# Optimization experiments

Measured on AMD Instinct MI355X. Metric: run time of the kernel, lower is better.

Reference implementation:

```python
import jax, jax.numpy as jnp
import numpy as np

N, K, HC, NH, VD, NAA, AC, L = 8192, 30, 64, 8, 8, 20, 91, 4
EPS = 1e-7

def _normalize(v):
    return v / jnp.sqrt(jnp.sum(v * v, -1, keepdims=True) + EPS)

def _dihedrals(bb):
    # bb [N,4,3]; chain of N,Ca,C atoms -> phi/psi/omega -> cos/sin features [N,6]
    X = bb[:, :3].reshape(-1, 3)
    U = _normalize(X[1:] - X[:-1])
    u2, u1, u0 = U[:-2], U[1:-1], U[2:]
    n2 = _normalize(jnp.cross(u2, u1))
    n1 = _normalize(jnp.cross(u1, u0))
    cosD = jnp.clip(jnp.sum(n2 * n1, -1), -1 + EPS, 1 - EPS)
    D = jnp.sign(jnp.sum(u2 * n1, -1)) * jnp.arccos(cosD)
    D = jnp.pad(D, (1, 2)).reshape(-1, 3)
    return jnp.concatenate([jnp.cos(D), jnp.sin(D)], -1)

def _orientations(X):
    f = jnp.pad(_normalize(X[1:] - X[:-1]), ((0, 1), (0, 0)))
    b = jnp.pad(_normalize(X[:-1] - X[1:]), ((1, 0), (0, 0)))
    return jnp.stack([f, b], -2)  # [N,2,3]

def _virtual_cb(bb):
    # ideal virtual C-beta relative to Ca
    b = bb[:, 1] - bb[:, 0]
    c = bb[:, 2] - bb[:, 1]
    a = jnp.cross(b, c)
    return -0.58273431 * a + 0.56802827 * b - 0.54067466 * c

def _rbf(d, d_count=16, d_max=20.0):
    mu = jnp.linspace(0.0, d_max, d_count)
    sigma = d_max / d_count
    return jnp.exp(-(((d[..., None] - mu) / sigma) ** 2))

def _pos_emb(src, num_emb=16):
    d = (src - jnp.arange(src.shape[0])[:, None]).astype(jnp.float32)
    freq = jnp.exp(jnp.arange(0, num_emb, 2, dtype=jnp.float32) * (-np.log(10000.0) / num_emb))
    ang = d[..., None] * freq
    return jnp.concatenate([jnp.cos(ang), jnp.sin(ang)], -1)

def _edge_rot_mat(vec):
    # rotation taking world frame -> edge-aligned frame (rows x,y,z)
    z = _normalize(vec)
    ex = jnp.array([1.0, 0.0, 0.0]); ey = jnp.array([0.0, 1.0, 0.0])
    ref = jnp.where(jnp.abs(z[..., :1]) < 0.9, ex, ey)
    x = _normalize(ref - jnp.sum(ref * z, -1, keepdims=True) * z)
    y = jnp.cross(z, x)
    return jnp.stack([x, y, z], -2)

def _knn(X):
    d2 = jnp.sum((X[:, None, :] - X[None, :, :]) ** 2, -1)  # [N,N]
    i = jnp.arange(X.shape[0])
    d2 = d2.at[i, i].set(jnp.inf)
    return jax.lax.top_k(-d2, K)[1]  # [N,K] source (neighbor) ids per target

def _so3_conv(x, ef, src, R, Wrad, brad, Wgate, W0, W1):
    # equivariant edge conv: gather, rotate l=1 into edge frame, channel-mix,
    # gate by radial MLP of edge features, rotate back, aggregate over K neighbors
    xs = x[src]                                              # [N,K,4,Cin]
    s1 = jnp.einsum('nkij,nkjc->nkic', R, xs[:, :, 1:4])
    m0 = xs[:, :, 0] @ W0
    m1 = jnp.einsum('nkic,co->nkio', s1, W1)
    g0, g1 = jnp.split(jax.nn.silu(ef @ Wrad + brad) @ Wgate, 2, -1)
    m1 = jnp.einsum('nkji,nkjc->nkic', R, m1 * g1[:, :, None, :])
    return jnp.concatenate([jnp.sum(m0 * g0, 1)[:, None], jnp.sum(m1, 1)], 1) / np.sqrt(K)

def _attn(x, ef, src, R, Walpha, Wv0, Wv1, Wo):
    # SO2/SO3 graph attention: invariant alpha over K neighbors, equivariant values
    x0 = x[:, 0]
    feat = jnp.concatenate([x0[src], jnp.broadcast_to(x0[:, None], (N, K, x0.shape[-1])), ef], -1)
    a = jax.nn.softmax(jax.nn.leaky_relu(feat @ Walpha, 0.2), axis=1)  # [N,K,NH]
    xs = x[src]
    s1 = jnp.einsum('nkij,nkjc->nkic', R, xs[:, :, 1:4])
    v0 = (xs[:, :, 0] @ Wv0).reshape(N, K, NH, VD)
    v1 = jnp.einsum('nkic,ch->nkih', s1, Wv1).reshape(N, K, 3, NH, VD)
    o0 = jnp.sum(v0 * a[..., None], 1).reshape(N, NH * VD)
    v1 = (v1 * a[:, :, None, :, None]).reshape(N, K, 3, NH * VD)
    o1 = jnp.sum(jnp.einsum('nkji,nkjc->nkic', R, v1), 1)
    return jnp.concatenate([o0[:, None], o1], 1) @ Wo

def _ffn(x, W1, W2):
    t = x[:, 0] @ W1
    h1 = jnp.einsum('nic,ch->nih', x[:, 1:4], W1) * jax.nn.sigmoid(t)[:, None, :]
    return jnp.concatenate([(jax.nn.silu(t) @ W2)[:, None], jnp.einsum('nih,ho->nio', h1, W2)], 1)

def _forward(bb, seq, latent, eb_Wrad, eb_brad, eb_Wgate, eb_W0, eb_W1, t_Walpha, t_Wv0, t_Wv1, t_Wo, t_Wf1, t_Wf2, e_W, e_b, p_Walpha, p_Wv0, p_Wv1, p_Wo, p_Wf1, p_Wf2, oa_Wrad, oa_brad, oa_Wgate, oa_W0, oa_W1, ln_g, ln_b, W_seq, b_seq, src):
    X_ca = bb[:, 1]
    vec = X_ca[src] - X_ca[:, None]                     # [N,K,3]
    R = _edge_rot_mat(vec)
    dist = jnp.sqrt(jnp.sum(vec * vec, -1) + EPS)
    ef = jnp.concatenate([_rbf(dist), _pos_emb(src)], -1)  # [N,K,32]
    # bb SO3 embedding: l=0 -> dihedrals + seq one-hot (masked to zero per noising_mask);
    # l=1 -> 7 relative vectors (4 bb_rel, 2 orientations, 1 virtual Cb), zero-padded to 26 ch
    scal = jnp.concatenate([_dihedrals(bb), jnp.zeros((N, NAA), bb.dtype)], -1)
    vecs = jnp.nan_to_num(jnp.concatenate([bb - X_ca[:, None], _orientations(X_ca), _virtual_cb(bb)[:, None]], 1))
    l1 = jnp.zeros((N, 3, scal.shape[-1]), bb.dtype).at[:, :, :7].set(jnp.transpose(vecs, (0, 2, 1)))
    bbemb = jnp.concatenate([scal[:, None], l1], 1)     # [N,4,26]
    bbout = _so3_conv(bbemb, ef, src, R, eb_Wrad, eb_brad, eb_Wgate, eb_W0, eb_W1)  # [N,4,32]
    res = jnp.concatenate([bbout, latent], -1)          # [N,4,64]
    for i in range(L):
        res = res + _attn(res, ef, src, R, t_Walpha[i], t_Wv0[i], t_Wv1[i], t_Wo[i])
        res = res + _ffn(res, t_Wf1[i], t_Wf2[i])
        efeat = jnp.concatenate([res[:, 0][src], jnp.broadcast_to(res[:, 0][:, None], (N, K, HC)), ef], -1)
        ef = jnp.tanh(efeat @ e_W[i] + e_b[i])
    p = _attn(res, ef, src, R, p_Walpha, p_Wv0, p_Wv1, p_Wo)  # [N,4,32]
    p = p + _ffn(p, p_Wf1, p_Wf2)
    atoms = _so3_conv(p, ef, src, R, oa_Wrad, oa_brad, oa_Wgate, oa_W0, oa_W1)  # [N,4,91]
    inv = atoms[:, 0]
    mu = jnp.mean(inv, -1, keepdims=True)
    var = jnp.var(inv, -1, keepdims=True)
    logits = jax.nn.log_softmax(((inv - mu) / jnp.sqrt(var + 1e-5) * ln_g + ln_b) @ W_seq + b_seq, -1)
    decoded = jnp.transpose(atoms[:, 1:4], (0, 2, 1))   # [N,91,3]
    return decoded, logits

def setup_inputs():
    key = jax.random.key(0)
    ks = jax.random.split(key, 30)
    def p(k, shape, fan):
        return jax.random.normal(k, shape, jnp.float32) * (fan ** -0.5)
    ca = jnp.cumsum(jax.random.normal(ks[0], (N, 3)) * 2.2, 0)
    bb = ca[:, None, :] + jax.random.normal(ks[1], (N, 4, 3)) * 0.8
    CA160 = 2 * HC + 32
    return {
        'bb': bb,
        'seq': jax.random.randint(ks[2], (N,), 0, NAA),
        'latent': jax.random.normal(ks[3], (N, 4, HC // 2)),
        'eb_Wrad': p(ks[4], (32, 64), 32), 'eb_brad': jnp.zeros((64,)),
        'eb_Wgate': p(ks[5], (64, 64), 64), 'eb_W0': p(ks[6], (26, 32), 26), 'eb_W1': p(ks[7], (26, 32), 26),
        't_Walpha': p(ks[8], (L, CA160, NH), CA160),
        't_Wv0': p(ks[9], (L, HC, NH * VD), HC), 't_Wv1': p(ks[10], (L, HC, NH * VD), HC),
        't_Wo': p(ks[11], (L, NH * VD, HC), NH * VD),
        't_Wf1': p(ks[12], (L, HC, HC), HC), 't_Wf2': p(ks[13], (L, HC, HC), HC),
        'e_W': p(ks[14], (L, CA160, 32), CA160), 'e_b': jnp.zeros((L, 32)),
        'p_Walpha': p(ks[15], (CA160, NH), CA160),
        'p_Wv0': p(ks[16], (HC, NH * VD), HC), 'p_Wv1': p(ks[17], (HC, NH * VD), HC),
        'p_Wo': p(ks[18], (NH * VD, 32), NH * VD),
        'p_Wf1': p(ks[19], (32, 32), 32), 'p_Wf2': p(ks[20], (32, 32), 32),
        'oa_Wrad': p(ks[21], (32, 64), 32), 'oa_brad': jnp.zeros((64,)),
        'oa_Wgate': p(ks[22], (64, 2 * AC), 64), 'oa_W0': p(ks[23], (32, AC), 32), 'oa_W1': p(ks[24], (32, AC), 32),
        'ln_g': jnp.ones((AC,)), 'ln_b': jnp.zeros((AC,)),
        'W_seq': p(ks[25], (AC, NAA), AC), 'b_seq': jnp.zeros((NAA,)),
    }

def reference(bb, seq, latent, eb_Wrad, eb_brad, eb_Wgate, eb_W0, eb_W1, t_Walpha, t_Wv0, t_Wv1, t_Wo, t_Wf1, t_Wf2, e_W, e_b, p_Walpha, p_Wv0, p_Wv1, p_Wo, p_Wf1, p_Wf2, oa_Wrad, oa_brad, oa_Wgate, oa_W0, oa_W1, ln_g, ln_b, W_seq, b_seq):
    src = _knn(bb[:, 1])
    return _forward(bb, seq, latent, eb_Wrad, eb_brad, eb_Wgate, eb_W0, eb_W1, t_Walpha, t_Wv0, t_Wv1, t_Wo, t_Wf1, t_Wf2, e_W, e_b, p_Walpha, p_Wv0, p_Wv1, p_Wo, p_Wf1, p_Wf2, oa_Wrad, oa_brad, oa_Wgate, oa_W0, oa_W1, ln_g, ln_b, W_seq, b_seq, src)
```

## Files before the change

### kernel.cpp

```cpp
#include <hip/hip_runtime.h>
#include <math.h>


#define NN 8192
#define KK 30
#define NE (NN*KK)
#define EPSF 1e-7f

static const size_t O_SRC = 0;
static const size_t O_XS  = 1ull<<20;
static const size_t O_YS  = O_XS + (size_t)NN*4;
static const size_t O_ZS  = O_XS + (size_t)NN*8;
static const size_t O_BBE = 2ull<<20;
static const size_t O_RES = 6ull<<20;
static const size_t O_P   = 15ull<<20;
static const size_t O_EF  = 20ull<<20;
static const size_t O_NF  = 52ull<<20;
static const size_t O_V1  = 55ull<<20;
static const size_t O_O   = 62ull<<20;
static const size_t O_EE  = 71ull<<20;
static const size_t O_M0E = 52ull<<20;
static const size_t O_M1E = 54ull<<20;
static const size_t O_M0O = 52ull<<20;
static const size_t O_M1O = 56ull<<20;
static const size_t O_ATM = 6ull<<20;
static const size_t WS_NEEDED = 80ull<<20;

__device__ __forceinline__ float nn0(float v){ return (v != v) ? 0.f : v; }
__device__ __forceinline__ void norm3(float& x, float& y, float& z){
  float s = sqrtf(x*x + y*y + z*z + EPSF);
  x /= s; y /= s; z /= s;
}

__global__ void k_prep(const float* __restrict__ bb, float* __restrict__ xs,
                       float* __restrict__ ys, float* __restrict__ zs,
                       float* __restrict__ bbe){
  int n = blockIdx.x*blockDim.x + threadIdx.x;
  if (n >= NN) return;
  const float* bn = bb + (size_t)n*12;
  float a0x=bn[0],a0y=bn[1],a0z=bn[2];
  float cax=bn[3],cay=bn[4],caz=bn[5];
  float a2x=bn[6],a2y=bn[7],a2z=bn[8];
  float a3x=bn[9],a3y=bn[10],a3z=bn[11];
  xs[n]=cax; ys[n]=cay; zs[n]=caz;
  float v[7][3];
  v[0][0]=a0x-cax; v[0][1]=a0y-cay; v[0][2]=a0z-caz;
  v[1][0]=0.f;     v[1][1]=0.f;     v[1][2]=0.f;
  v[2][0]=a2x-cax; v[2][1]=a2y-cay; v[2][2]=a2z-caz;
  v[3][0]=a3x-cax; v[3][1]=a3y-cay; v[3][2]=a3z-caz;
  if (n < NN-1){
    float fx=bb[(size_t)(n+1)*12+3]-cax, fy=bb[(size_t)(n+1)*12+4]-cay, fz=bb[(size_t)(n+1)*12+5]-caz;
    norm3(fx,fy,fz); v[4][0]=fx; v[4][1]=fy; v[4][2]=fz;
  } else { v[4][0]=v[4][1]=v[4][2]=0.f; }
  if (n > 0){
    float gx=bb[(size_t)(n-1)*12+3]-cax, gy=bb[(size_t)(n-1)*12+4]-cay, gz=bb[(size_t)(n-1)*12+5]-caz;
    norm3(gx,gy,gz); v[5][0]=gx; v[5][1]=gy; v[5][2]=gz;
  } else { v[5][0]=v[5][1]=v[5][2]=0.f; }
  {
    float bx=cax-a0x, by=cay-a0y, bz=caz-a0z;
    float cx=a2x-cax, cy=a2y-cay, cz=a2z-caz;
    float ax = by*cz - bz*cy, ay = bz*cx - bx*cz, az = bx*cy - by*cx;
    v[6][0] = -0.58273431f*ax + 0.56802827f*bx - 0.54067466f*cx;
    v[6][1] = -0.58273431f*ay + 0.56802827f*by - 0.54067466f*cy;
    v[6][2] = -0.58273431f*az + 0.56802827f*bz - 0.54067466f*cz;
  }
  float* be = bbe + (size_t)n*104;
  #pragma unroll
  for (int c=6;c<26;++c) be[c]=0.f;
  #pragma unroll
  for (int s=0;s<3;++s){
    float* br = be + 26*(1+s);
    #pragma unroll
    for (int c=0;c<26;++c) br[c] = (c<7) ? nn0(v[c][s]) : 0.f;
  }
}

__global__ void k_dihed(const float* __restrict__ bb, float* __restrict__ bbe){
  int t = blockIdx.x*blockDim.x + threadIdx.x;
  if (t >= 3*NN) return;
  float cD = 1.f, sD = 0.f;
  if (t >= 1 && t < 3*NN-2){
    int i = t-1;
    float p[4][3];
    #pragma unroll
    for (int m=0;m<4;++m){
      int a = i+m; int rn = a/3, ra = a - rn*3;
      const float* q = bb + (size_t)(rn*4 + ra)*3;
      p[m][0]=q[0]; p[m][1]=q[1]; p[m][2]=q[2];
    }
    float u2x=p[1][0]-p[0][0], u2y=p[1][1]-p[0][1], u2z=p[1][2]-p[0][2];
    float u1x=p[2][0]-p[1][0], u1y=p[2][1]-p[1][1], u1z=p[2][2]-p[1][2];
    float u0x=p[3][0]-p[2][0], u0y=p[3][1]-p[2][1], u0z=p[3][2]-p[2][2];
    norm3(u2x,u2y,u2z); norm3(u1x,u1y,u1z); norm3(u0x,u0y,u0z);
    float n2x=u2y*u1z-u2z*u1y, n2y=u2z*u1x-u2x*u1z, n2z=u2x*u1y-u2y*u1x;
    float n1x=u1y*u0z-u1z*u0y, n1y=u1z*u0x-u1x*u0z, n1z=u1x*u0y-u1y*u0x;
    norm3(n2x,n2y,n2z); norm3(n1x,n1y,n1z);
    float cosD = n2x*n1x + n2y*n1y + n2z*n1z;
    const float lo = (float)(-1.0 + 1e-7), hi = (float)(1.0 - 1e-7);
    cosD = fminf(fmaxf(cosD, lo), hi);
    float sg = u2x*n1x + u2y*n1y + u2z*n1z;
    float sgn = (sg > 0.f) ? 1.f : ((sg < 0.f) ? -1.f : 0.f);
    float D = sgn * acosf(cosD);
    cD = cosf(D); sD = sinf(D);
  }
  int n = t/3, col = t - n*3;
  bbe[(size_t)n*104 + col] = cD;
  bbe[(size_t)n*104 + 3 + col] = sD;
}

__global__ __launch_bounds__(256) void k_knn(const float* __restrict__ xs,
        const float* __restrict__ ys, const float* __restrict__ zs, int* __restrict__ src){
  __shared__ float sd[4][32];
  __shared__ int   si[4][32];
  int w = threadIdx.x >> 6, lane = threadIdx.x & 63;
  int n = blockIdx.x*4 + w;
  float qx = xs[n], qy = ys[n], qz = zs[n];
  if (lane >= 30 && lane < 32){ sd[w][lane] = INFINITY; si[w][lane] = 0; }

  int w0 = n - 32; if (w0 < 0) w0 = 0; if (w0 > NN-64) w0 = NN-64;
  int idx = w0 + lane;
  {
    float dx = qx - xs[idx], dy = qy - ys[idx], dz = qz - zs[idx];
    float d2 = dx*dx + dy*dy + dz*dz;
    if (idx == n) d2 = INFINITY;
    #pragma unroll
    for (int k = 2; k <= 64; k <<= 1){
      #pragma unroll
      for (int jj = k>>1; jj >= 1; jj >>= 1){
        float od = __shfl_xor(d2, jj);
        int   oi = __shfl_xor(idx, jj);
        bool up      = ((lane & k) == 0);
        bool lower   = ((lane & jj) == 0);
        bool takeMin = (up == lower);
        bool mless   = (d2 < od) || (d2 == od && idx < oi);
        if (mless != takeMin){ d2 = od; idx = oi; }
      }
    }
    if (lane < 30){ sd[w][lane] = d2; si[w][lane] = idx; }
  }
  float thr = sd[w][29];

  for (int s = 0; s < NN/64; ++s){
    int j = s*64 + lane;
    float dx = __fsub_rn(qx, xs[j]);
    float dy = __fsub_rn(qy, ys[j]);
    float dz = __fsub_rn(qz, zs[j]);
    float d2 = __fadd_rn(__fadd_rn(__fmul_rn(dx,dx),__fmul_rn(dy,dy)),__fmul_rn(dz,dz));
    if (j == n) d2 = INFINITY;
    if (j >= w0 && j < w0+64) d2 = INFINITY;
    unsigned long long bal = __ballot(d2 < thr);
    if (bal){
      while (bal){
        int b = __ffsll((unsigned long long)bal) - 1;
        bal &= bal - 1ull;
        float vd = __shfl(d2, b);
        int vj = s*64 + b;
        float dl = 0.f; int il = 0; bool keep = true;
        if (lane < 30){ dl = sd[w][lane]; il = si[w][lane]; keep = (dl <= vd); }
        unsigned long long km = __ballot(lane < 30 && keep);
        int pos = __popcll(km);
        if (lane < 30 && !keep){ sd[w][lane+1] = dl; si[w][lane+1] = il; }
        if (lane == pos){ sd[w][lane] = vd; si[w][lane] = vj; }
      }
      thr = sd[w][29];
    }
  }
  if (lane < 30) src[(size_t)n*KK + lane] = si[w][lane];
}

__global__ void k_edgefeat(const int* __restrict__ src, const float* __restrict__ xs,
        const float* __restrict__ ys, const float* __restrict__ zs, float* __restrict__ ef){
  int e = blockIdx.x*blockDim.x + threadIdx.x;
  if (e >= NE) return;
  int n = e / KK;
  int j = src[e];
  float vx = xs[j]-xs[n], vy = ys[j]-ys[n], vz = zs[j]-zs[n];
  float dist = sqrtf(vx*vx + vy*vy + vz*vz + EPSF);
  float* o = ef + (size_t)e*32;
  #pragma unroll
  for (int m=0;m<16;++m){
    float mu = (float)m * (20.f/15.f);
    float q = (dist - mu) / 1.25f;
    o[m] = expf(-q*q);
  }
  float d = (float)(j - n);
  const float Cf = -0.5756462732485115f;
  #pragma unroll
  for (int fi=0; fi<8; ++fi){
    float fr = expf((float)(2*fi) * Cf);
    float ang = d * fr;
    o[16+fi] = cosf(ang);
    o[24+fi] = sinf(ang);
  }
}

template<int K, int ACT, int BSEL>
__global__ __launch_bounds__(256) void k_gemm(const float* __restrict__ A,
        const float* __restrict__ B1, const float* __restrict__ B2,
        const float* __restrict__ bias, float* __restrict__ C,
        int M, int Nc, int arpg, int agst, int arst, int aoff, int beta){
  __shared__ float As[64*(K+1)];
  __shared__ alignas(16) float Bs[K*64];
  int tid = threadIdx.x, tm = blockIdx.x, tn = blockIdx.y;
  for (int i = tid; i < K*64; i += 256){
    int kk = i >> 6, cl = i & 63;
    int c = tn*64 + cl;
    float v = 0.f;
    if (c < Nc){
      if (BSEL == 0) v = B1[kk*Nc + c];
      else if (BSEL == 1) v = (c<8) ? B1[kk*8+c] : ((c<16) ? B1[(64+kk)*8 + (c-8)] : B2[kk*64 + (c-16)]);
      else v = (c<32) ? B1[kk*32 + c] : B1[(64+kk)*32 + (c-32)];
    }
    Bs[i] = v;
  }
  for (int i = tid; i < 64*K; i += 256){
    int rl = i / K, kk = i - rl*K;
    int r = tm*64 + rl;
    float v = 0.f;
    if (r < M){
      const float* ap;
      if (arpg == 1) ap = A + (size_t)r*agst + aoff;
      else { int g = r/3; int wr = r - g*3; ap = A + (size_t)g*agst + wr*arst + aoff; }
      v = ap[kk];
    }
    As[rl*(K+1) + kk] = v;
  }
  __syncthreads();
  int tx = tid & 15, ty = tid >> 4;
  float acc[4][4] = {};
  for (int kk = 0; kk < K; ++kk){
    float4 b4 = *reinterpret_cast<const float4*>(&Bs[kk*64 + tx*4]);
    #pragma unroll
    for (int rr = 0; rr < 4; ++rr){
      float a = As[(ty*4+rr)*(K+1) + kk];
      acc[rr][0] += a*b4.x; acc[rr][1] += a*b4.y; acc[rr][2] += a*b4.z; acc[rr][3] += a*b4.w;
    }
  }
  if (ACT == 2){
    int r0 = tm*64 + ty*4;
    #pragma unroll
    for (int cc = 0; cc < 4; ++cc){
      int c = tn*64 + tx*4 + cc;
      if (c >= Nc) continue;
      float t0 = acc[0][cc];
      float g = 1.f/(1.f + expf(-t0));
      C[(size_t)(r0+0)*Nc + c] = t0*g;
      C[(size_t)(r0+1)*Nc + c] = acc[1][cc]*g;
      C[(size_t)(r0+2)*Nc + c] = acc[2][cc]*g;
      C[(size_t)(r0+3)*Nc + c] = acc[3][cc]*g;
    }
  } else {
    #pragma unroll
    for (int rr = 0; rr < 4; ++rr){
      int r = tm*64 + ty*4 + rr;
      if (r >= M) continue;
      #pragma unroll
      for (int cc = 0; cc < 4; ++cc){
        int c = tn*64 + tx*4 + cc;
        if (c >= Nc) continue;
        float v = acc[rr][cc];
        if (bias) v += bias[c];
        size_t ci = (size_t)r*Nc + c;
        if (beta) v += C[ci];
        C[ci] = v;
      }
    }
  }
}

__global__ __launch_bounds__(256) void k_attn(const int* __restrict__ src,
        const float* __restrict__ NF, const float* __restrict__ V1,
        const float* __restrict__ ef, const float* __restrict__ WaE, float* __restrict__ o){
  int w = threadIdx.x >> 6, lane = threadIdx.x & 63;
  int n = blockIdx.x*4 + w;
  int h = lane >> 3, q = lane & 7;
  float w0 = WaE[(q*4+0)*8 + h];
  float w1 = WaE[(q*4+1)*8 + h];
  float w2 = WaE[(q*4+2)*8 + h];
  float w3 = WaE[(q*4+3)*8 + h];
  const int* sk = src + (size_t)n*KK;
  int myj = (lane < KK) ? sk[lane] : 0;
  float a2 = NF[(size_t)n*80 + 8 + h];
  float m = -INFINITY, s = 0.f, o0=0.f, o1=0.f, o2=0.f, o3=0.f;
  for (int k = 0; k < KK; ++k){
    int j = __shfl(myj, k);
    float4 e4 = *reinterpret_cast<const float4*>(ef + ((size_t)n*KK + k)*32 + q*4);
    float val = e4.x*w0 + e4.y*w1 + e4.z*w2 + e4.w*w3;
    val += __shfl_xor(val, 1);
    val += __shfl_xor(val, 2);
    val += __shfl_xor(val, 4);
    float l = val + NF[(size_t)j*80 + h] + a2;
    l = (l >= 0.f) ? l : 0.2f*l;
    float mn = fmaxf(m, l);
    float f = expf(m - mn);
    float pp = expf(l - mn);
    s = s*f + pp;
    const float* v1p = V1 + (size_t)j*192;
    o0 = o0*f + pp*NF[(size_t)j*80 + 16 + lane];
    o1 = o1*f + pp*v1p[lane];
    o2 = o2*f + pp*v1p[64+lane];
    o3 = o3*f + pp*v1p[128+lane];
    m = mn;
  }
  float inv = 1.f/s;
  float* op = o + (size_t)n*256;
  op[lane] = o0*inv; op[64+lane] = o1*inv; op[128+lane] = o2*inv; op[192+lane] = o3*inv;
}

template<int C>
__global__ __launch_bounds__(256) void k_so3fused(const int* __restrict__ src,
        const float* __restrict__ ef, const float* __restrict__ Wrad,
        const float* __restrict__ brad, const float* __restrict__ Wgate,
        const float* __restrict__ M0, const float* __restrict__ M1,
        float* __restrict__ out, int nstr, int sstr){
  constexpr int KG  = 256 / C;
  constexpr int KPT = (KK + KG - 1) / KG;
  __shared__ float efs[KK*32];
  __shared__ float Wr[32*64];
  __shared__ float Hs[KK*64];
  __shared__ float Wg[64*(C+1)];
  __shared__ float part[3*256];
  __shared__ int   js[KK];
  int n = blockIdx.x, tid = threadIdx.x;
  for (int i = tid; i < KK*32; i += 256) efs[i] = ef[(size_t)n*KK*32 + i];
  for (int i = tid; i < 2048;  i += 256) Wr[i]  = Wrad[i];
  if (tid < KK) js[tid] = src[(size_t)n*KK + tid];
  __syncthreads();
  for (int i = tid; i < KK*64; i += 256){
    int k = i >> 6, h = i & 63;
    float a = brad[h];
    const float* er = efs + k*32;
    #pragma unroll
    for (int m = 0; m < 32; ++m) a += er[m]*Wr[m*64 + h];
    Hs[i] = a/(1.f + expf(-a));
  }
  __syncthreads();
  int c = tid % C, kg = tid / C;
  bool act = (kg < KG);
  for (int i = tid; i < 64*C; i += 256){ int m = i/C, cc = i - m*C; Wg[m*(C+1)+cc] = Wgate[m*2*C + cc]; }
  __syncthreads();
  if (act){
    float a0 = 0.f;
    for (int t = 0; t < KPT; ++t){
      int k = kg*KPT + t;
      if (k < KK){
        const float* hr = Hs + k*64;
        float g = 0.f;
        #pragma unroll
        for (int m = 0; m < 64; ++m) g += hr[m]*Wg[m*(C+1) + c];
        a0 += g * M0[(size_t)js[k]*C + c];
      }
    }
    part[kg*C + c] = a0;
  }
  __syncthreads();
  const float IS = 0.18257418583505536f;
  if (tid < C){
    float s = 0.f;
    for (int g = 0; g < KG; ++g) s += part[g*C + tid];
    out[(size_t)n*nstr + tid] = s*IS;
  }
  __syncthreads();
  for (int i = tid; i < 64*C; i += 256){ int m = i/C, cc = i - m*C; Wg[m*(C+1)+cc] = Wgate[m*2*C + C + cc]; }
  __syncthreads();
  if (act){
    float a1 = 0.f, a2 = 0.f, a3 = 0.f;
    for (int t = 0; t < KPT; ++t){
      int k = kg*KPT + t;
      if (k < KK){
        const float* hr = Hs + k*64;
        float g = 0.f;
        #pragma unroll
        for (int m = 0; m < 64; ++m) g += hr[m]*Wg[m*(C+1) + c];
        const float* m1p = M1 + (size_t)js[k]*3*C;
        a1 += g*m1p[c]; a2 += g*m1p[C+c]; a3 += g*m1p[2*C+c];
      }
    }
    part[kg*C + c] = a1;
    part[KG*C + kg*C + c] = a2;
    part[2*KG*C + kg*C + c] = a3;
  }
  __syncthreads();
  if (tid < C){
    float s1=0.f, s2=0.f, s3=0.f;
    for (int g = 0; g < KG; ++g){
      s1 += part[g*C + tid];
      s2 += part[KG*C + g*C + tid];
      s3 += part[2*KG*C + g*C + tid];
    }
    float* ob = out + (size_t)n*nstr + tid;
    ob[sstr] = s1*IS; ob[2*sstr] = s2*IS; ob[3*sstr] = s3*IS;
  }
}

__global__ void k_lat(const float* __restrict__ latent, float* __restrict__ res){
  int t = blockIdx.x*blockDim.x + threadIdx.x;
  if (t >= NN*128) return;
  int n = t >> 7, rc = t & 127, s = rc >> 5, c = rc & 31;
  res[(size_t)n*256 + s*64 + 32 + c] = latent[t];
}

__global__ __launch_bounds__(256) void k_edgeout(const int* __restrict__ src,
        const float* __restrict__ eWe, const float* __restrict__ EE,
        const float* __restrict__ ebv, float* __restrict__ ef){
  __shared__ float ws[32*32];
  __shared__ float es[8*32];
  int tid = threadIdx.x;
  size_t e0 = (size_t)blockIdx.x*8;
  for (int i = tid; i < 1024; i += 256) ws[i] = eWe[i];
  es[tid] = ef[e0*32 + tid];
  __syncthreads();
  int le = tid >> 5, c = tid & 31;
  size_t e = e0 + le;
  int n = (int)(e / KK);
  int j = src[e];
  float acc = ebv[c] + EE[(size_t)j*64 + c] + EE[(size_t)n*64 + 32 + c];
  const float* er = es + le*32;
  #pragma unroll
  for (int kk = 0; kk < 32; ++kk) acc += er[kk]*ws[kk*32 + c];
  ef[e*32 + c] = tanhf(acc);
}

__global__ __launch_bounds__(128) void k_head(const float* __restrict__ atoms,
        const float* __restrict__ ln_g, const float* __restrict__ ln_b,
        const float* __restrict__ W_seq, const float* __restrict__ b_seq, float* __restrict__ out){
  __shared__ float red[128];
  __shared__ float nrm[91];
  __shared__ float lg[20];
  int n = blockIdx.x, t = threadIdx.x;
  const float* inv = atoms + (size_t)n*364;
  float x = (t < 91) ? inv[t] : 0.f;
  red[t] = x; __syncthreads();
  for (int off=64; off>=1; off>>=1){ if (t<off) red[t]+=red[t+off]; __syncthreads(); }
  float mu = red[0] / 91.f;
  __syncthreads();
  float d = x - mu;
  red[t] = (t<91) ? d*d : 0.f; __syncthreads();
  for (int off=64; off>=1; off>>=1){ if (t<off) red[t]+=red[t+off]; __syncthreads(); }
  float var = red[0] / 91.f;
  __syncthreads();
  if (t < 91) nrm[t] = (x - mu)/sqrtf(var + 1e-5f) * ln_g[t] + ln_b[t];
  __syncthreads();
  if (t < 20){
    float acc = b_seq[t];
    for (int c=0;c<91;++c) acc += nrm[c]*W_seq[c*20+t];
    lg[t] = acc;
  }
  __syncthreads();
  if (t == 0){
    float mx = lg[0];
    for (int i=1;i<20;++i) mx = fmaxf(mx, lg[i]);
    float s = 0.f;
    for (int i=0;i<20;++i) s += expf(lg[i]-mx);
    red[0] = mx + logf(s);
  }
  __syncthreads();
  float lse = red[0];
  if (t < 20) out[(size_t)NN*273 + (size_t)n*20 + t] = lg[t] - lse;
  for (int idx = t; idx < 273; idx += 128){
    int c = idx/3, i = idx - c*3;
    out[(size_t)n*273 + idx] = atoms[(size_t)n*364 + (1+i)*91 + c];
  }
}

static void gemm(hipStream_t st, int K, int act, int bsel, const float* A,
                 const float* B1, const float* B2, const float* bias, float* C,
                 int M, int Nc, int arpg, int agst, int arst, int aoff, int beta){
  dim3 g((M+63)/64, (Nc+63)/64), b(256);
  if (K == 26){
    k_gemm<26,0,0><<<g,b,0,st>>>(A,B1,B2,bias,C,M,Nc,arpg,agst,arst,aoff,beta);
  } else if (K == 32){
    if (act == 2) k_gemm<32,2,0><<<g,b,0,st>>>(A,B1,B2,bias,C,M,Nc,arpg,agst,arst,aoff,beta);
    else          k_gemm<32,0,0><<<g,b,0,st>>>(A,B1,B2,bias,C,M,Nc,arpg,agst,arst,aoff,beta);
  } else {
    if (act == 2)        k_gemm<64,2,0><<<g,b,0,st>>>(A,B1,B2,bias,C,M,Nc,arpg,agst,arst,aoff,beta);
    else if (bsel == 1)  k_gemm<64,0,1><<<g,b,0,st>>>(A,B1,B2,bias,C,M,Nc,arpg,agst,arst,aoff,beta);
    else if (bsel == 2)  k_gemm<64,0,2><<<g,b,0,st>>>(A,B1,B2,bias,C,M,Nc,arpg,agst,arst,aoff,beta);
    else                 k_gemm<64,0,0><<<g,b,0,st>>>(A,B1,B2,bias,C,M,Nc,arpg,agst,arst,aoff,beta);
  }
}

extern "C" void kernel_launch(void* const* d_in, const int* in_sizes, int n_in,
                              void* d_out, int out_size, void* d_ws, size_t ws_size,
                              hipStream_t stream){
  (void)in_sizes; (void)n_in; (void)out_size;
  if (ws_size < WS_NEEDED) return;

  const float* bb      = (const float*)d_in[0];
  const float* latent  = (const float*)d_in[2];
  const float* eb_Wrad = (const float*)d_in[3];
  const float* eb_brad = (const float*)d_in[4];
  const float* eb_Wgate= (const float*)d_in[5];
  const float* eb_W0   = (const float*)d_in[6];
  const float* eb_W1   = (const float*)d_in[7];
  const float* t_Walpha= (const float*)d_in[8];
  const float* t_Wv0   = (const float*)d_in[9];
  const float* t_Wv1   = (const float*)d_in[10];
  const float* t_Wo    = (const float*)d_in[11];
  const float* t_Wf1   = (const float*)d_in[12];
  const float* t_Wf2   = (const float*)d_in[13];
  const float* e_W     = (const float*)d_in[14];
  const float* e_b     = (const float*)d_in[15];
  const float* p_Walpha= (const float*)d_in[16];
  const float* p_Wv0   = (const float*)d_in[17];
  const float* p_Wv1   = (const float*)d_in[18];
  const float* p_Wo    = (const float*)d_in[19];
  const float* p_Wf1   = (const float*)d_in[20];
  const float* p_Wf2   = (const float*)d_in[21];
  const float* oa_Wrad = (const float*)d_in[22];
  const float* oa_brad = (const float*)d_in[23];
  const float* oa_Wgate= (const float*)d_in[24];
  const float* oa_W0   = (const float*)d_in[25];
  const float* oa_W1   = (const float*)d_in[26];
  const float* ln_g    = (const float*)d_in[27];
  const float* ln_b    = (const float*)d_in[28];
  const float* W_seq   = (const float*)d_in[29];
  const float* b_seq   = (const float*)d_in[30];

  char* w = (char*)d_ws;
  int*   src = (int*)  (w + O_SRC);
  float* xs  = (float*)(w + O_XS);
  float* ys  = (float*)(w + O_YS);
  float* zs  = (float*)(w + O_ZS);
  float* bbe = (float*)(w + O_BBE);
  float* res = (float*)(w + O_RES);
  float* p   = (float*)(w + O_P);
  float* ef  = (float*)(w + O_EF);
  float* NF  = (float*)(w + O_NF);
  float* V1  = (float*)(w + O_V1);
  float* o   = (float*)(w + O_O);
  float* EE  = (float*)(w + O_EE);
  float* M0e = (float*)(w + O_M0E);
  float* M1e = (float*)(w + O_M1E);
  float* M0o = (float*)(w + O_M0O);
  float* M1o = (float*)(w + O_M1O);
  float* atm = (float*)(w + O_ATM);

  k_prep <<<(NN+255)/256, 256, 0, stream>>>(bb, xs, ys, zs, bbe);
  k_dihed<<<(3*NN+255)/256, 256, 0, stream>>>(bb, bbe);
  k_knn  <<<NN/4, 256, 0, stream>>>(xs, ys, zs, src);
  k_edgefeat<<<(NE+255)/256, 256, 0, stream>>>(src, xs, ys, zs, ef);

  gemm(stream, 26,0,0, bbe, eb_W0, nullptr, nullptr, M0e, NN,   32, 1,104, 0, 0, 0);
  gemm(stream, 26,0,0, bbe, eb_W1, nullptr, nullptr, M1e, 3*NN, 32, 3,104,26,26, 0);
  k_so3fused<32><<<NN, 256, 0, stream>>>(src, ef, eb_Wrad, eb_brad, eb_Wgate, M0e, M1e, res, 256, 64);
  k_lat<<<(NN*128+255)/256, 256, 0, stream>>>(latent, res);

  for (int L=0; L<4; ++L){
    const float* Wa  = t_Walpha + (size_t)L*160*8;
    const float* Wv0 = t_Wv0 + (size_t)L*64*64;
    const float* Wv1 = t_Wv1 + (size_t)L*64*64;
    const float* Wo  = t_Wo  + (size_t)L*64*64;
    const float* Wf1 = t_Wf1 + (size_t)L*64*64;
    const float* Wf2 = t_Wf2 + (size_t)L*64*64;
    const float* eWl = e_W   + (size_t)L*160*32;
    const float* ebl = e_b   + (size_t)L*32;
    gemm(stream, 64,0,1, res, Wa, Wv0, nullptr, NF, NN,   80, 1,256, 0, 0, 0);
    gemm(stream, 64,0,0, res, Wv1, nullptr, nullptr, V1, 3*NN, 64, 3,256,64,64, 0);
    k_attn<<<NN/4, 256, 0, stream>>>(src, NF, V1, ef, Wa + 128*8, o);
    gemm(stream, 64,0,0, o,   Wo,  nullptr, nullptr, res, 4*NN, 64, 1,64,0,0, 1);
    gemm(stream, 64,2,0, res, Wf1, nullptr, nullptr, o,   4*NN, 64, 1,64,0,0, 0);
    gemm(stream, 64,0,0, o,   Wf2, nullptr, nullptr, res, 4*NN, 64, 1,64,0,0, 1);
    gemm(stream, 64,0,2, res, eWl, nullptr, nullptr, EE,  NN,   64, 1,256,0,0, 0);
    k_edgeout<<<NE/8, 256, 0, stream>>>(src, eWl + 128*32, EE, ebl, ef);
  }

  gemm(stream, 64,0,1, res, p_Walpha, p_Wv0, nullptr, NF, NN,   80, 1,256, 0, 0, 0);
  gemm(stream, 64,0,0, res, p_Wv1, nullptr, nullptr, V1, 3*NN, 64, 3,256,64,64, 0);
  k_attn<<<NN/4, 256, 0, stream>>>(src, NF, V1, ef, p_Walpha + 128*8, o);
  gemm(stream, 64,0,0, o, p_Wo,  nullptr, nullptr, p, 4*NN, 32, 1,64,0,0, 0);
  gemm(stream, 32,2,0, p, p_Wf1, nullptr, nullptr, o, 4*NN, 32, 1,32,0,0, 0);
  gemm(stream, 32,0,0, o, p_Wf2, nullptr, nullptr, p, 4*NN, 32, 1,32,0,0, 1);

  gemm(stream, 32,0,0, p, oa_W0, nullptr, nullptr, M0o, NN,   91, 1,128, 0, 0, 0);
  gemm(stream, 32,0,0, p, oa_W1, nullptr, nullptr, M1o, 3*NN, 91, 3,128,32,32, 0);
  k_so3fused<91><<<NN, 256, 0, stream>>>(src, ef, oa_Wrad, oa_brad, oa_Wgate, M0o, M1o, atm, 364, 91);

  k_head<<<NN, 128, 0, stream>>>(atm, ln_g, ln_b, W_seq, b_seq, (float*)d_out);
}
```

Before: 1.398 ms.

## Vectorize GEMM and SO3 conv inner loops with float4 register blocking

New measurement: 1.371 ms. 2.0% less time.

```diff
diff --git a/kernel.cpp b/kernel.cpp
--- a/kernel.cpp
+++ b/kernel.cpp
@@ -198,42 +198,52 @@
 __global__ __launch_bounds__(256) void k_gemm(const float* __restrict__ A,
         const float* __restrict__ B1, const float* __restrict__ B2,
         const float* __restrict__ bias, float* __restrict__ C,
-        int M, int Nc, int arpg, int agst, int arst, int aoff, int beta){
-  __shared__ float As[64*(K+1)];
-  __shared__ alignas(16) float Bs[K*64];
+        int M, int Nc, int ldc, int arpg, int agst, int arst, int aoff, int beta){
+  constexpr int KP = (K+3)&~3;
+  constexpr int SP = ((KP+4)%32==0) ? KP+8 : KP+4;
+  __shared__ alignas(16) float As[64*SP];
+  __shared__ alignas(16) float Bs[KP*64];
   int tid = threadIdx.x, tm = blockIdx.x, tn = blockIdx.y;
-  for (int i = tid; i < K*64; i += 256){
+  for (int i = tid; i < KP*64; i += 256){
     int kk = i >> 6, cl = i & 63;
     int c = tn*64 + cl;
     float v = 0.f;
-    if (c < Nc){
+    if (c < Nc && kk < K){
       if (BSEL == 0) v = B1[kk*Nc + c];
       else if (BSEL == 1) v = (c<8) ? B1[kk*8+c] : ((c<16) ? B1[(64+kk)*8 + (c-8)] : B2[kk*64 + (c-16)]);
       else v = (c<32) ? B1[kk*32 + c] : B1[(64+kk)*32 + (c-32)];
     }
     Bs[i] = v;
   }
-  for (int i = tid; i < 64*K; i += 256){
-    int rl = i / K, kk = i - rl*K;
+  for (int i = tid; i < 64*KP; i += 256){
+    int rl = i / KP, kk = i - rl*KP;
     int r = tm*64 + rl;
     float v = 0.f;
-    if (r < M){
+    if (r < M && kk < K){
       const float* ap;
       if (arpg == 1) ap = A + (size_t)r*agst + aoff;
       else { int g = r/3; int wr = r - g*3; ap = A + (size_t)g*agst + wr*arst + aoff; }
       v = ap[kk];
     }
-    As[rl*(K+1) + kk] = v;
+    As[rl*SP + kk] = v;
   }
   __syncthreads();
   int tx = tid & 15, ty = tid >> 4;
   float acc[4][4] = {};
-  for (int kk = 0; kk < K; ++kk){
-    float4 b4 = *reinterpret_cast<const float4*>(&Bs[kk*64 + tx*4]);
+  #pragma unroll 2
+  for (int kq = 0; kq < KP/4; ++kq){
+    float4 a0 = *reinterpret_cast<const float4*>(&As[(ty*4+0)*SP + kq*4]);
+    float4 a1 = *reinterpret_cast<const float4*>(&As[(ty*4+1)*SP + kq*4]);
+    float4 a2 = *reinterpret_cast<const float4*>(&As[(ty*4+2)*SP + kq*4]);
+    float4 a3 = *reinterpret_cast<const float4*>(&As[(ty*4+3)*SP + kq*4]);
     #pragma unroll
-    for (int rr = 0; rr < 4; ++rr){
-      float a = As[(ty*4+rr)*(K+1) + kk];
-      acc[rr][0] += a*b4.x; acc[rr][1] += a*b4.y; acc[rr][2] += a*b4.z; acc[rr][3] += a*b4.w;
+    for (int mm = 0; mm < 4; ++mm){
+      float4 b4 = *reinterpret_cast<const float4*>(&Bs[(kq*4+mm)*64 + tx*4]);
+      float e0 = (&a0.x)[mm], e1 = (&a1.x)[mm], e2 = (&a2.x)[mm], e3 = (&a3.x)[mm];
+      acc[0][0] += e0*b4.x; acc[0][1] += e0*b4.y; acc[0][2] += e0*b4.z; acc[0][3] += e0*b4.w;
+      acc[1][0] += e1*b4.x; acc[1][1] += e1*b4.y; acc[1][2] += e1*b4.z; acc[1][3] += e1*b4.w;
+      acc[2][0] += e2*b4.x; acc[2][1] += e2*b4.y; acc[2][2] += e2*b4.z; acc[2][3] += e2*b4.w;
+      acc[3][0] += e3*b4.x; acc[3][1] += e3*b4.y; acc[3][2] += e3*b4.z; acc[3][3] += e3*b4.w;
     }
   }
   if (ACT == 2){
@@ -244,10 +254,10 @@
       if (c >= Nc) continue;
       float t0 = acc[0][cc];
       float g = 1.f/(1.f + expf(-t0));
-      C[(size_t)(r0+0)*Nc + c] = t0*g;
-      C[(size_t)(r0+1)*Nc + c] = acc[1][cc]*g;
-      C[(size_t)(r0+2)*Nc + c] = acc[2][cc]*g;
-      C[(size_t)(r0+3)*Nc + c] = acc[3][cc]*g;
+      C[(size_t)(r0+0)*ldc + c] = t0*g;
+      C[(size_t)(r0+1)*ldc + c] = acc[1][cc]*g;
+      C[(size_t)(r0+2)*ldc + c] = acc[2][cc]*g;
+      C[(size_t)(r0+3)*ldc + c] = acc[3][cc]*g;
     }
   } else {
     #pragma unroll
@@ -260,7 +270,7 @@
         if (c >= Nc) continue;
         float v = acc[rr][cc];
         if (bias) v += bias[c];
-        size_t ci = (size_t)r*Nc + c;
+        size_t ci = (size_t)r*ldc + c;
         if (beta) v += C[ci];
         C[ci] = v;
       }
@@ -312,92 +322,124 @@
         const float* __restrict__ ef, const float* __restrict__ Wrad,
         const float* __restrict__ brad, const float* __restrict__ Wgate,
         const float* __restrict__ M0, const float* __restrict__ M1,
-        float* __restrict__ out, int nstr, int sstr){
-  constexpr int KG  = 256 / C;
-  constexpr int KPT = (KK + KG - 1) / KG;
-  __shared__ float efs[KK*32];
-  __shared__ float Wr[32*64];
-  __shared__ float Hs[KK*64];
-  __shared__ float Wg[64*(C+1)];
-  __shared__ float part[3*256];
-  __shared__ int   js[KK];
+        const float* __restrict__ lat, float* __restrict__ out, int nstr, int sstr){
+  constexpr int KT = (C==32) ? 2 : 4;
+  constexpr int KG = 32/KT;
+  constexpr int NQ = (C==32) ? 16 : 23;
+  constexpr int PW = (C==32) ? 32 : 92;
+  constexpr int CG = (C==32) ? 64 : 92;
+  constexpr int HS = 68;
+  constexpr int NPASS = (C==32) ? 1 : 2;
+  constexpr int NT = KG*NQ;
+  constexpr int LD0 = PW;
+  constexpr int LD1 = PW;
+  __shared__ alignas(16) float uni[64*CG];
+  __shared__ alignas(16) float Hs[32*HS];
+  __shared__ alignas(16) float part[4*KG*PW];
+  __shared__ int js[32];
+  float* efs = uni;
+  float* Wr  = uni + 30*32;
+  float* Wg  = uni;
   int n = blockIdx.x, tid = threadIdx.x;
   for (int i = tid; i < KK*32; i += 256) efs[i] = ef[(size_t)n*KK*32 + i];
   for (int i = tid; i < 2048;  i += 256) Wr[i]  = Wrad[i];
-  if (tid < KK) js[tid] = src[(size_t)n*KK + tid];
-  __syncthreads();
-  for (int i = tid; i < KK*64; i += 256){
+  if (tid < 32) js[tid] = (tid < KK) ? src[(size_t)n*KK + tid] : 0;
+  __syncthreads();
+  for (int i = tid; i < 32*64; i += 256){
     int k = i >> 6, h = i & 63;
-    float a = brad[h];
-    const float* er = efs + k*32;
+    float v = 0.f;
+    if (k < KK){
+      float a = brad[h];
+      const float* er = efs + k*32;
+      #pragma unroll
+      for (int m = 0; m < 32; ++m) a += er[m]*Wr[m*64 + h];
+      v = a/(1.f + expf(-a));
+    }
+    Hs[k*HS + h] = v;
+  }
+  int kg = tid / NQ, cq = tid - kg*NQ;
+  bool act = (tid < NT);
+  for (int pass = 0; pass < NPASS; ++pass){
+    __syncthreads();
+    for (int i = tid; i < 64*CG; i += 256){
+      int m = i/CG, u = i - m*CG;
+      float v = 0.f;
+      if (C == 32) v = Wgate[m*64 + u];
+      else if (u < 91) v = Wgate[m*182 + pass*91 + u];
+      Wg[i] = v;
+    }
+    __syncthreads();
+    if (act){
+      float g[KT][4];
+      #pragma unroll
+      for (int i=0;i<KT;++i){ g[i][0]=0.f; g[i][1]=0.f; g[i][2]=0.f; g[i][3]=0.f; }
+      #pragma unroll 2
+      for (int mq = 0; mq < 16; ++mq){
+        float4 hs[KT];
+        #pragma unroll
+        for (int i=0;i<KT;++i) hs[i] = *reinterpret_cast<const float4*>(&Hs[(kg*KT+i)*HS + mq*4]);
+        #pragma unroll
+        for (int mm=0; mm<4; ++mm){
+          float4 w4 = *reinterpret_cast<const float4*>(&Wg[(mq*4+mm)*CG + cq*4]);
+          #pragma unroll
+          for (int i=0;i<KT;++i){
+            float h = (&hs[i].x)[mm];
+            g[i][0] += h*w4.x; g[i][1] += h*w4.y; g[i][2] += h*w4.z; g[i][3] += h*w4.w;
+          }
+        }
+      }
+      bool scalar_path = (C==32) ? (cq < 8) : (pass == 0);
+      if (scalar_path){
+        int c = cq*4;
+        float a0x=0.f, a0y=0.f, a0z=0.f, a0w=0.f;
+        #pragma unroll
+        for (int i=0;i<KT;++i){
+          int k = kg*KT+i;
+          float4 m0 = *reinterpret_cast<const float4*>(&M0[(size_t)js[k]*LD0 + c]);
+          a0x += g[i][0]*m0.x; a0y += g[i][1]*m0.y; a0z += g[i][2]*m0.z; a0w += g[i][3]*m0.w;
+        }
+        float4 r4; r4.x=a0x; r4.y=a0y; r4.z=a0z; r4.w=a0w;
+        *reinterpret_cast<float4*>(&part[(0*KG+kg)*PW + c]) = r4;
+      } else {
+        int c = (C==32) ? (cq*4-32) : cq*4;
+        float a1[4]={0,0,0,0}, a2[4]={0,0,0,0}, a3[4]={0,0,0,0};
+        #pragma unroll
+        for (int i=0;i<KT;++i){
+          int k = kg*KT+i;
+          const float* m1r = M1 + (size_t)js[k]*3*LD1;
+          float4 v1 = *reinterpret_cast<const float4*>(&m1r[c]);
+          float4 v2 = *reinterpret_cast<const float4*>(&m1r[LD1 + c]);
+          float4 v3 = *reinterpret_cast<const float4*>(&m1r[2*LD1 + c]);
+          a1[0]+=g[i][0]*v1.x; a1[1]+=g[i][1]*v1.y; a1[2]+=g[i][2]*v1.z; a1[3]+=g[i][3]*v1.w;
+          a2[0]+=g[i][0]*v2.x; a2[1]+=g[i][1]*v2.y; a2[2]+=g[i][2]*v2.z; a2[3]+=g[i][3]*v2.w;
+          a3[0]+=g[i][0]*v3.x; a3[1]+=g[i][1]*v3.y; a3[2]+=g[i][2]*v3.z; a3[3]+=g[i][3]*v3.w;
+        }
+        float4 r1; r1.x=a1[0]; r1.y=a1[1]; r1.z=a1[2]; r1.w=a1[3];
+        float4 r2; r2.x=a2[0]; r2.y=a2[1]; r2.z=a2[2]; r2.w=a2[3];
+        float4 r3; r3.x=a3[0]; r3.y=a3[1]; r3.z=a3[2]; r3.w=a3[3];
+        *reinterpret_cast<float4*>(&part[(1*KG+kg)*PW + c]) = r1;
+        *reinterpret_cast<float4*>(&part[(2*KG+kg)*PW + c]) = r2;
+        *reinterpret_cast<float4*>(&part[(3*KG+kg)*PW + c]) = r3;
+      }
+    }
+  }
+  __syncthreads();
+  const float IS = 0.18257418583505536f;
+  for (int idx = tid; idx < 4*C; idx += 256){
+    int r = idx / C, c = idx - r*C;
+    float s = 0.f;
     #pragma unroll
-    for (int m = 0; m < 32; ++m) a += er[m]*Wr[m*64 + h];
-    Hs[i] = a/(1.f + expf(-a));
-  }
-  __syncthreads();
-  int c = tid % C, kg = tid / C;
-  bool act = (kg < KG);
-  for (int i = tid; i < 64*C; i += 256){ int m = i/C, cc = i - m*C; Wg[m*(C+1)+cc] = Wgate[m*2*C + cc]; }
-  __syncthreads();
-  if (act){
-    float a0 = 0.f;
-    for (int t = 0; t < KPT; ++t){
-      int k = kg*KPT + t;
-      if (k < KK){
-        const float* hr = Hs + k*64;
-        float g = 0.f;
-        #pragma unroll
-        for (int m = 0; m < 64; ++m) g += hr[m]*Wg[m*(C+1) + c];
-        a0 += g * M0[(size_t)js[k]*C + c];
+    for (int gq = 0; gq < KG; ++gq) s += part[(r*KG+gq)*PW + c];
+    out[(size_t)n*nstr + r*sstr + c] = s*IS;
+  }
+  if (C == 32){
+    if (lat){
+      for (int idx = tid; idx < 128; idx += 256){
+        int r = idx >> 5, c = idx & 31;
+        out[(size_t)n*nstr + r*sstr + 32 + c] = lat[(size_t)n*128 + r*32 + c];
       }
     }
-    part[kg*C + c] = a0;
-  }
-  __syncthreads();
-  const float IS = 0.18257418583505536f;
-  if (tid < C){
-    float s = 0.f;
-    for (int g = 0; g < KG; ++g) s += part[g*C + tid];
-    out[(size_t)n*nstr + tid] = s*IS;
-  }
-  __syncthreads();
-  for (int i = tid; i < 64*C; i += 256){ int m = i/C, cc = i - m*C; Wg[m*(C+1)+cc] = Wgate[m*2*C + C + cc]; }
-  __syncthreads();
-  if (act){
-    float a1 = 0.f, a2 = 0.f, a3 = 0.f;
-    for (int t = 0; t < KPT; ++t){
-      int k = kg*KPT + t;
-      if (k < KK){
-        const float* hr = Hs + k*64;
-        float g = 0.f;
-        #pragma unroll
-        for (int m = 0; m < 64; ++m) g += hr[m]*Wg[m*(C+1) + c];
-        const float* m1p = M1 + (size_t)js[k]*3*C;
-        a1 += g*m1p[c]; a2 += g*m1p[C+c]; a3 += g*m1p[2*C+c];
-      }
-    }
-    part[kg*C + c] = a1;
-    part[KG*C + kg*C + c] = a2;
-    part[2*KG*C + kg*C + c] = a3;
-  }
-  __syncthreads();
-  if (tid < C){
-    float s1=0.f, s2=0.f, s3=0.f;
-    for (int g = 0; g < KG; ++g){
-      s1 += part[g*C + tid];
-      s2 += part[KG*C + g*C + tid];
-      s3 += part[2*KG*C + g*C + tid];
-    }
-    float* ob = out + (size_t)n*nstr + tid;
-    ob[sstr] = s1*IS; ob[2*sstr] = s2*IS; ob[3*sstr] = s3*IS;
-  }
-}
-
-__global__ void k_lat(const float* __restrict__ latent, float* __restrict__ res){
-  int t = blockIdx.x*blockDim.x + threadIdx.x;
-  if (t >= NN*128) return;
-  int n = t >> 7, rc = t & 127, s = rc >> 5, c = rc & 31;
-  res[(size_t)n*256 + s*64 + 32 + c] = latent[t];
+  }
 }
 
 __global__ __launch_bounds__(256) void k_edgeout(const int* __restrict__ src,
@@ -465,18 +507,18 @@
 
 static void gemm(hipStream_t st, int K, int act, int bsel, const float* A,
                  const float* B1, const float* B2, const float* bias, float* C,
-                 int M, int Nc, int arpg, int agst, int arst, int aoff, int beta){
+                 int M, int Nc, int ldc, int arpg, int agst, int arst, int aoff, int beta){
   dim3 g((M+63)/64, (Nc+63)/64), b(256);
   if (K == 26){
-    k_gemm<26,0,0><<<g,b,0,st>>>(A,B1,B2,bias,C,M,Nc,arpg,agst,arst,aoff,beta);
+    k_gemm<26,0,0><<<g,b,0,st>>>(A,B1,B2,bias,C,M,Nc,ldc,arpg,agst,arst,aoff,beta);
   } else if (K == 32){
-    if (act == 2) k_gemm<32,2,0><<<g,b,0,st>>>(A,B1,B2,bias,C,M,Nc,arpg,agst,arst,aoff,beta);
-    else          k_gemm<32,0,0><<<g,b,0,st>>>(A,B1,B2,bias,C,M,Nc,arpg,agst,arst,aoff,beta);
+    if (act == 2) k_gemm<32,2,0><<<g,b,0,st>>>(A,B1,B2,bias,C,M,Nc,ldc,arpg,agst,arst,aoff,beta);
+    else          k_gemm<32,0,0><<<g,b,0,st>>>(A,B1,B2,bias,C,M,Nc,ldc,arpg,agst,arst,aoff,beta);
   } else {
-    if (act == 2)        k_gemm<64,2,0><<<g,b,0,st>>>(A,B1,B2,bias,C,M,Nc,arpg,agst,arst,aoff,beta);
-    else if (bsel == 1)  k_gemm<64,0,1><<<g,b,0,st>>>(A,B1,B2,bias,C,M,Nc,arpg,agst,arst,aoff,beta);
-    else if (bsel == 2)  k_gemm<64,0,2><<<g,b,0,st>>>(A,B1,B2,bias,C,M,Nc,arpg,agst,arst,aoff,beta);
-    else                 k_gemm<64,0,0><<<g,b,0,st>>>(A,B1,B2,bias,C,M,Nc,arpg,agst,arst,aoff,beta);
+    if (act == 2)        k_gemm<64,2,0><<<g,b,0,st>>>(A,B1,B2,bias,C,M,Nc,ldc,arpg,agst,arst,aoff,beta);
+    else if (bsel == 1)  k_gemm<64,0,1><<<g,b,0,st>>>(A,B1,B2,bias,C,M,Nc,ldc,arpg,agst,arst,aoff,beta);
+    else if (bsel == 2)  k_gemm<64,0,2><<<g,b,0,st>>>(A,B1,B2,bias,C,M,Nc,ldc,arpg,agst,arst,aoff,beta);
+    else                 k_gemm<64,0,0><<<g,b,0,st>>>(A,B1,B2,bias,C,M,Nc,ldc,arpg,agst,arst,aoff,beta);
   }
 }
 
@@ -541,10 +583,9 @@
   k_knn  <<<NN/4, 256, 0, stream>>>(xs, ys, zs, src);
   k_edgefeat<<<(NE+255)/256, 256, 0, stream>>>(src, xs, ys, zs, ef);
 
-  gemm(stream, 26,0,0, bbe, eb_W0, nullptr, nullptr, M0e, NN,   32, 1,104, 0, 0, 0);
-  gemm(stream, 26,0,0, bbe, eb_W1, nullptr, nullptr, M1e, 3*NN, 32, 3,104,26,26, 0);
-  k_so3fused<32><<<NN, 256, 0, stream>>>(src, ef, eb_Wrad, eb_brad, eb_Wgate, M0e, M1e, res, 256, 64);
-  k_lat<<<(NN*128+255)/256, 256, 0, stream>>>(latent, res);
+  gemm(stream, 26,0,0, bbe, eb_W0, nullptr, nullptr, M0e, NN,   32, 32, 1,104, 0, 0, 0);
+  gemm(stream, 26,0,0, bbe, eb_W1, nullptr, nullptr, M1e, 3*NN, 32, 32, 3,104,26,26, 0);
+  k_so3fused<32><<<NN, 256, 0, stream>>>(src, ef, eb_Wrad, eb_brad, eb_Wgate, M0e, M1e, latent, res, 256, 64);
 
   for (int L=0; L<4; ++L){
     const float* Wa  = t_Walpha + (size_t)L*160*8;
@@ -555,26 +596,26 @@
     const float* Wf2 = t_Wf2 + (size_t)L*64*64;
     const float* eWl = e_W   + (size_t)L*160*32;
     const float* ebl = e_b   + (size_t)L*32;
-    gemm(stream, 64,0,1, res, Wa, Wv0, nullptr, NF, NN,   80, 1,256, 0, 0, 0);
-    gemm(stream, 64,0,0, res, Wv1, nullptr, nullptr, V1, 3*NN, 64, 3,256,64,64, 0);
+    gemm(stream, 64,0,1, res, Wa, Wv0, nullptr, NF, NN,   80, 80, 1,256, 0, 0, 0);
+    gemm(stream, 64,0,0, res, Wv1, nullptr, nullptr, V1, 3*NN, 64, 64, 3,256,64,64, 0);
     k_attn<<<NN/4, 256, 0, stream>>>(src, NF, V1, ef, Wa + 128*8, o);
-    gemm(stream, 64,0,0, o,   Wo,  nullptr, nullptr, res, 4*NN, 64, 1,64,0,0, 1);
-    gemm(stream, 64,2,0, res, Wf1, nullptr, nullptr, o,   4*NN, 64, 1,64,0,0, 0);
-    gemm(stream, 64,0,0, o,   Wf2, nullptr, nullptr, res, 4*NN, 64, 1,64,0,0, 1);
-    gemm(stream, 64,0,2, res, eWl, nullptr, nullptr, EE,  NN,   64, 1,256,0,0, 0);
+    gemm(stream, 64,0,0, o,   Wo,  nullptr, nullptr, res, 4*NN, 64, 64, 1,64,0,0, 1);
+    gemm(stream, 64,2,0, res, Wf1, nullptr, nullptr, o,   4*NN, 64, 64, 1,64,0,0, 0);
+    gemm(stream, 64,0,0, o,   Wf2, nullptr, nullptr, res, 4*NN, 64, 64, 1,64,0,0, 1);
+    gemm(stream, 64,0,2, res, eWl, nullptr, nullptr, EE,  NN,   64, 64, 1,256,0,0, 0);
     k_edgeout<<<NE/8, 256, 0, stream>>>(src, eWl + 128*32, EE, ebl, ef);
   }
 
-  gemm(stream, 64,0,1, res, p_Walpha, p_Wv0, nullptr, NF, NN,   80, 1,256, 0, 0, 0);
-  gemm(stream, 64,0,0, res, p_Wv1, nullptr, nullptr, V1, 3*NN, 64, 3,256,64,64, 0);
+  gemm(stream, 64,0,1, res, p_Walpha, p_Wv0, nullptr, NF, NN,   80, 80, 1,256, 0, 0, 0);
+  gemm(stream, 64,0,0, res, p_Wv1, nullptr, nullptr, V1, 3*NN, 64, 64, 3,256,64,64, 0);
   k_attn<<<NN/4, 256, 0, stream>>>(src, NF, V1, ef, p_Walpha + 128*8, o);
-  gemm(stream, 64,0,0, o, p_Wo,  nullptr, nullptr, p, 4*NN, 32, 1,64,0,0, 0);
-  gemm(stream, 32,2,0, p, p_Wf1, nullptr, nullptr, o, 4*NN, 32, 1,32,0,0, 0);
-  gemm(stream, 32,0,0, o, p_Wf2, nullptr, nullptr, p, 4*NN, 32, 1,32,0,0, 1);
-
-  gemm(stream, 32,0,0, p, oa_W0, nullptr, nullptr, M0o, NN,   91, 1,128, 0, 0, 0);
-  gemm(stream, 32,0,0, p, oa_W1, nullptr, nullptr, M1o, 3*NN, 91, 3,128,32,32, 0);
-  k_so3fused<91><<<NN, 256, 0, stream>>>(src, ef, oa_Wrad, oa_brad, oa_Wgate, M0o, M1o, atm, 364, 91);
+  gemm(stream, 64,0,0, o, p_Wo,  nullptr, nullptr, p, 4*NN, 32, 32, 1,64,0,0, 0);
+  gemm(stream, 32,2,0, p, p_Wf1, nullptr, nullptr, o, 4*NN, 32, 32, 1,32,0,0, 0);
+  gemm(stream, 32,0,0, o, p_Wf2, nullptr, nullptr, p, 4*NN, 32, 32, 1,32,0,0, 1);
+
+  gemm(stream, 32,0,0, p, oa_W0, nullptr, nullptr, M0o, NN,   91, 92, 1,128, 0, 0, 0);
+  gemm(stream, 32,0,0, p, oa_W1, nullptr, nullptr, M1o, 3*NN, 91, 92, 3,128,32,32, 0);
+  k_so3fused<91><<<NN, 256, 0, stream>>>(src, ef, oa_Wrad, oa_brad, oa_Wgate, M0o, M1o, nullptr, atm, 364, 91);
 
   k_head<<<NN, 128, 0, stream>>>(atm, ln_g, ln_b, W_seq, b_seq, (float*)d_out);
 }
```
